# Optimization experiments

Hardware: AMD Instinct MI355X
Metric: run time of the kernel (lower is better)

Reference implementation:

```python
import jax, jax.numpy as jnp
import numpy as np

NUM_HEADS = 8

def setup_inputs() -> dict:
    key = jax.random.key(0)
    ks = jax.random.split(key, 12)
    B, C, H, W = 4, 256, 64, 64
    QK = 256
    NSP = 256
    x = jax.random.normal(ks[0], (B, C, H, W), dtype=jnp.float32)
    affinity_matrix = jax.random.uniform(ks[1], (B, NSP, H * W), dtype=jnp.float32)
    norm_w = 1.0 + 0.02 * jax.random.normal(ks[2], (C,), dtype=jnp.float32)
    norm_b = 0.02 * jax.random.normal(ks[3], (C,), dtype=jnp.float32)
    Wq = 0.02 * jax.random.normal(ks[4], (QK, C), dtype=jnp.float32)
    Wk = 0.02 * jax.random.normal(ks[5], (QK, C), dtype=jnp.float32)
    Wv = 0.02 * jax.random.normal(ks[6], (C, C), dtype=jnp.float32)
    Wsp = 0.02 * jax.random.normal(ks[7], (QK, C), dtype=jnp.float32)
    lepe_w = 0.02 * jax.random.normal(ks[8], (C, 1, 3, 3), dtype=jnp.float32)  # depthwise OIHW
    lepe_b = 0.02 * jax.random.normal(ks[9], (C,), dtype=jnp.float32)
    return {"x": x, "affinity_matrix": affinity_matrix, "norm_w": norm_w,
            "norm_b": norm_b, "Wq": Wq, "Wk": Wk, "Wv": Wv, "Wsp": Wsp,
            "lepe_w": lepe_w, "lepe_b": lepe_b, "num_spixels": NSP}


def _layernorm2d(x, w, b, eps=1e-6):
    # LayerNorm over channel dim of NCHW input
    xp = x.transpose(0, 2, 3, 1)  # B,H,W,C
    mu = xp.mean(-1, keepdims=True)
    var = ((xp - mu) ** 2).mean(-1, keepdims=True)
    xn = (xp - mu) * jax.lax.rsqrt(var + eps) * w + b
    return xn.transpose(0, 3, 1, 2)


def _sgca(x, affinity_matrix, norm_w, norm_b, Wq, Wk, Wv, Wsp, lepe_w, lepe_b, num_spixels):
    B, C, H, W = x.shape
    HW = H * W
    h = NUM_HEADS
    qk_dim = Wq.shape[0]
    dqk = qk_dim // h
    dv = C // h
    scale = (C // h) ** -0.5

    xn = _layernorm2d(x, norm_w, norm_b)

    # superpixel aggregation: b (hw) c
    x_flat = xn.reshape(B, C, HW).transpose(0, 2, 1)  # B,HW,C
    stoken = jnp.einsum('bmn,bnc->bmc', affinity_matrix, x_flat)
    stoken = stoken / (affinity_matrix.sum(-1, keepdims=True) + 1e-16)  # B,nsp,C

    # sp projection -> B,h,dqk,nsp
    st = jnp.einsum('bmc,qc->bmq', stoken, Wsp).transpose(0, 2, 1)
    st = st.reshape(B, h, dqk, num_spixels)

    # 1x1 conv projections
    q = jnp.einsum('oc,bchw->bohw', Wq, xn).reshape(B, h, dqk, HW)
    k = jnp.einsum('oc,bchw->bohw', Wk, xn).reshape(B, h, dqk, HW)
    vx = jnp.einsum('oc,bchw->bohw', Wv, xn)  # B,C,H,W
    v = vx.reshape(B, h, dv, HW)

    # LePE: depthwise 3x3 conv on v(x)
    lepe = jax.lax.conv_general_dilated(
        vx, lepe_w, window_strides=(1, 1), padding=((1, 1), (1, 1)),
        feature_group_count=C, dimension_numbers=('NCHW', 'OIHW', 'NCHW'))
    lepe = lepe + lepe_b[None, :, None, None]
    # faithful to original: [B,C,HW] -> permute -> [B,HW,C] -> reshape B,C,H,W
    lepe = lepe.reshape(B, C, HW).transpose(0, 2, 1).reshape(B, C, H, W)

    # stage 1: k^T @ stoken, softmax over HW axis
    s_attn = jnp.einsum('bhdn,bhdm->bhnm', k, st) * scale  # B,h,HW,nsp
    s_attn = jax.nn.softmax(s_attn, axis=-2)
    s_out = jnp.einsum('bhdn,bhnm->bhdm', v, s_attn)  # B,h,dv,nsp

    # stage 2: stoken^T @ q, softmax over nsp axis
    x_attn = jnp.einsum('bhdm,bhdn->bhmn', st, q) * scale  # B,h,nsp,HW
    x_attn = jax.nn.softmax(x_attn, axis=-2)
    x_out = jnp.einsum('bhdm,bhmn->bhdn', s_out, x_attn).reshape(B, C, H, W)

    return x_out + lepe


def reference(x, affinity_matrix, norm_w, norm_b, Wq, Wk, Wv, Wsp, lepe_w, lepe_b, num_spixels):
    return _sgca(x, affinity_matrix, norm_w, norm_b, Wq, Wk, Wv, Wsp, lepe_w, lepe_b, num_spixels)
```

## Files before the change

kernel.cpp:

```cpp
#include <hip/hip_runtime.h>
#include <hip/hip_bf16.h>

#define BATCH 4
#define CCH   256
#define HWHW  4096
#define NSP   256
#define NHEAD 8
#define SCALE 0.17677669529663689f
#define PLANE 1048576L

typedef short bf16x8 __attribute__((ext_vector_type(8)));
typedef short bf16x4 __attribute__((ext_vector_type(4)));
typedef float f32x4  __attribute__((ext_vector_type(4)));

__device__ __forceinline__ short f2bs(float f) {
    __hip_bfloat16 h = __float2bfloat16(f);
    return *(short*)&h;
}
__device__ __forceinline__ bf16x8 cvt8(float4 a, float4 b) {
    bf16x8 p;
    p[0] = f2bs(a.x); p[1] = f2bs(a.y); p[2] = f2bs(a.z); p[3] = f2bs(a.w);
    p[4] = f2bs(b.x); p[5] = f2bs(b.y); p[6] = f2bs(b.z); p[7] = f2bs(b.w);
    return p;
}
__device__ __forceinline__ void gll16(const __hip_bfloat16* g, __hip_bfloat16* l) {
    __builtin_amdgcn_global_load_lds(
        (const __attribute__((address_space(1))) unsigned int*)(const void*)g,
        (__attribute__((address_space(3))) unsigned int*)(void*)l,
        16, 0, 0);
}

__global__ __launch_bounds__(512)
void ln_fused_kernel(const float* __restrict__ x, const float* __restrict__ w,
                     const float* __restrict__ bb,
                     const float* __restrict__ Wq, const float* __restrict__ Wk,
                     const float* __restrict__ Wv, const float* __restrict__ Wsp,
                     __hip_bfloat16* __restrict__ xn_cn,
                     __hip_bfloat16* __restrict__ xn_nc,
                     __hip_bfloat16* __restrict__ wbf)
{
    __shared__ float ps[32][64], pss[32][64];
    __shared__ float mus[64], rstds[64];
    __shared__ float wls[256], bls[256];
    int blk = blockIdx.x;
    int t = threadIdx.x;
    if (blk >= 256) {
        int sel = blk - 256;
        const float* src = (sel == 0) ? Wq : (sel == 1) ? Wk : (sel == 2) ? Wv : Wsp;
        __hip_bfloat16* dst = wbf + sel * 65536;
        for (int i = t * 4; i < 65536; i += 2048) {
            float4 f = *(const float4*)(src + i);
            __hip_bfloat16 p[4];
            p[0] = __float2bfloat16(f.x); p[1] = __float2bfloat16(f.y);
            p[2] = __float2bfloat16(f.z); p[3] = __float2bfloat16(f.w);
            *(int2*)(dst + i) = *(int2*)p;
        }
        return;
    }
    int b = blk >> 6;
    int n0 = (blk & 63) * 64;
    int pg = t & 15;
    int cq = t >> 4;
    if (t < 256) { wls[t] = w[t]; bls[t] = bb[t]; }

    const float* xp = x + ((long)(b * CCH + cq * 8)) * HWHW + n0 + pg * 4;
    float4 v[8];
#pragma unroll
    for (int i = 0; i < 8; ++i) v[i] = *(const float4*)(xp + (long)i * HWHW);
    float4 s = {0.f,0.f,0.f,0.f}, ss = {0.f,0.f,0.f,0.f};
#pragma unroll
    for (int i = 0; i < 8; ++i) {
        s.x += v[i].x; s.y += v[i].y; s.z += v[i].z; s.w += v[i].w;
        ss.x += v[i].x * v[i].x; ss.y += v[i].y * v[i].y;
        ss.z += v[i].z * v[i].z; ss.w += v[i].w * v[i].w;
    }
    *(float4*)&ps[cq][pg * 4]  = s;
    *(float4*)&pss[cq][pg * 4] = ss;
    __syncthreads();
    if (t < 64) {
        float S = 0.f, SS = 0.f;
#pragma unroll
        for (int q = 0; q < 32; ++q) { S += ps[q][t]; SS += pss[q][t]; }
        float mu = S * (1.f / 256.f);
        float var = SS * (1.f / 256.f) - mu * mu;
        mus[t] = mu; rstds[t] = rsqrtf(var + 1e-6f);
    }
    __syncthreads();
    float4 mu4 = *(float4*)&mus[pg * 4];
    float4 rs4 = *(float4*)&rstds[pg * 4];

    bf16x8 pk[4];
#pragma unroll
    for (int i = 0; i < 8; ++i) {
        int c = cq * 8 + i;
        float wc = wls[c], bc = bls[c];
        short h0 = f2bs((v[i].x - mu4.x) * rs4.x * wc + bc);
        short h1 = f2bs((v[i].y - mu4.y) * rs4.y * wc + bc);
        short h2 = f2bs((v[i].z - mu4.z) * rs4.z * wc + bc);
        short h3 = f2bs((v[i].w - mu4.w) * rs4.w * wc + bc);
        pk[0][i] = h0; pk[1][i] = h1; pk[2][i] = h2; pk[3][i] = h3;
        bf16x4 q; q[0] = h0; q[1] = h1; q[2] = h2; q[3] = h3;
        *(bf16x4*)(xn_cn + ((long)(b * CCH + c)) * HWHW + n0 + pg * 4) = q;
    }
#pragma unroll
    for (int j = 0; j < 4; ++j)
        *(bf16x8*)(xn_nc + ((long)b * HWHW + n0 + pg * 4 + j) * CCH + cq * 8) = pk[j];
}

__device__ __forceinline__ void gemm_k256_128(
    const __hip_bfloat16* __restrict__ A, const __hip_bfloat16* __restrict__ B,
    __hip_bfloat16* __restrict__ C, int bx, int by, int bz,
    int N, long aStrideZ, long bStrideZ, long cStrideZ,
    __hip_bfloat16* __restrict__ Asm)
{
    const int K = 256;
    const int t = threadIdx.x, lane = t & 63, w = t >> 6;
    const int l15 = lane & 15, quad = lane >> 4;
    const int Mt = by * 128, Nt = bx * 128;
    {
        const __hip_bfloat16* aBase = A + (long)bz * aStrideZ
            + (long)(Mt + l15) * K + quad * 8;
#pragma unroll
        for (int p = 0; p < 16; ++p) {
            const int rt = w * 2 + (p >> 3), s = p & 7;
            gll16(aBase + (long)(rt * 16) * K + s * 32, Asm + (rt * 8 + s) * 512);
        }
    }
    const int wm2 = w & 1, wn2 = w >> 1;
    const __hip_bfloat16* bBase = B + (long)bz * bStrideZ
        + (long)(Nt + wn2 * 64 + l15) * K + quad * 8;

    f32x4 acc[4][4];
#pragma unroll
    for (int mi = 0; mi < 4; ++mi)
#pragma unroll
        for (int nj = 0; nj < 4; ++nj) acc[mi][nj] = f32x4{0.f,0.f,0.f,0.f};

    bf16x8 bEv[4], bOd[4];
#pragma unroll
    for (int nj = 0; nj < 4; ++nj)
        bEv[nj] = *(const bf16x8*)(bBase + (long)(nj * 16) * K);
    __syncthreads();
#pragma unroll
    for (int sp = 0; sp < 4; ++sp) {
        const int s0 = 2 * sp, s1 = 2 * sp + 1;
#pragma unroll
        for (int nj = 0; nj < 4; ++nj)
            bOd[nj] = *(const bf16x8*)(bBase + (long)(nj * 16) * K + s1 * 32);
#pragma unroll
        for (int mi = 0; mi < 4; ++mi) {
            bf16x8 a = *(const bf16x8*)&Asm[((wm2 * 4 + mi) * 8 + s0) * 512 + lane * 8];
            acc[mi][0] = __builtin_amdgcn_mfma_f32_16x16x32_bf16(a, bEv[0], acc[mi][0], 0, 0, 0);
            acc[mi][1] = __builtin_amdgcn_mfma_f32_16x16x32_bf16(a, bEv[1], acc[mi][1], 0, 0, 0);
            acc[mi][2] = __builtin_amdgcn_mfma_f32_16x16x32_bf16(a, bEv[2], acc[mi][2], 0, 0, 0);
            acc[mi][3] = __builtin_amdgcn_mfma_f32_16x16x32_bf16(a, bEv[3], acc[mi][3], 0, 0, 0);
        }
        if (sp < 3) {
#pragma unroll
            for (int nj = 0; nj < 4; ++nj)
                bEv[nj] = *(const bf16x8*)(bBase + (long)(nj * 16) * K + (s0 + 2) * 32);
        }
#pragma unroll
        for (int mi = 0; mi < 4; ++mi) {
            bf16x8 a = *(const bf16x8*)&Asm[((wm2 * 4 + mi) * 8 + s1) * 512 + lane * 8];
            acc[mi][0] = __builtin_amdgcn_mfma_f32_16x16x32_bf16(a, bOd[0], acc[mi][0], 0, 0, 0);
            acc[mi][1] = __builtin_amdgcn_mfma_f32_16x16x32_bf16(a, bOd[1], acc[mi][1], 0, 0, 0);
            acc[mi][2] = __builtin_amdgcn_mfma_f32_16x16x32_bf16(a, bOd[2], acc[mi][2], 0, 0, 0);
            acc[mi][3] = __builtin_amdgcn_mfma_f32_16x16x32_bf16(a, bOd[3], acc[mi][3], 0, 0, 0);
        }
    }
#pragma unroll
    for (int mi = 0; mi < 4; ++mi)
#pragma unroll
        for (int nj = 0; nj < 4; ++nj)
#pragma unroll
            for (int r = 0; r < 4; ++r) {
                int m = Mt + wm2 * 64 + mi * 16 + quad * 4 + r;
                int n = Nt + wn2 * 64 + nj * 16 + l15;
                C[(long)bz * cStrideZ + (long)m * N + n] =
                    __float2bfloat16(acc[mi][nj][r]);
            }
}

template <int OUTK, int ASTAGE, bool ROWSUM, int NTL>
__device__ __forceinline__ void gemm_body(
    const void* __restrict__ Av, const __hip_bfloat16* __restrict__ B,
    void* __restrict__ Cptr, int bx, int by, int bz,
    int N, int K, int kChunk, int kShift,
    long aStrideZ, long bStrideZ, long cStrideZ,
    float* __restrict__ rsPart,
    __hip_bfloat16* __restrict__ Asm, __hip_bfloat16* __restrict__ Bsm,
    float* __restrict__ rsl)
{
    int z = bz;
    int b = z >> kShift;
    int ch = z & ((1 << kShift) - 1);
    int t = threadIdx.x;
    int lane = t & 63, w = t >> 6;
    int l15 = lane & 15, quad = lane >> 4;
    int Mt = by * 64, Nt = bx * 64 * NTL;

    if (ASTAGE == 2 && t < 64) {
        float s = 0.f;
#pragma unroll
        for (int pl = 0; pl < 8; ++pl) s += rsPart[((b * 8 + pl) << 8) + Mt + t];
        rsl[t] = s;
    }

    long aOff = (long)b * aStrideZ + (long)ch * kChunk
        + (long)(Mt + w * 16 + l15) * K + quad * 8;
    const float* aSrcF = (const float*)Av + aOff;
    const __hip_bfloat16* bSrc = B + (long)b * bStrideZ + (long)ch * kChunk
        + (long)(Nt + w * 16 + l15) * K + quad * 8;

    f32x4 acc[NTL][2][2];
#pragma unroll
    for (int nt = 0; nt < NTL; ++nt)
#pragma unroll
        for (int i = 0; i < 2; ++i)
#pragma unroll
            for (int j = 0; j < 2; ++j) acc[nt][i][j] = f32x4{0.f,0.f,0.f,0.f};
    f32x4 rs0 = {0.f,0.f,0.f,0.f}, rs1 = rs0;
    bf16x8 onesf;
    { short o = (l15 == 0) ? (short)0x3F80 : (short)0;
      onesf = bf16x8{o, o, o, o, o, o, o, o}; }
    int wm = (w & 1) * 2, wn = (w >> 1) * 2;

    float4 pf0, pf1, pf2, pf3;
    if (ASTAGE == 1) {
        pf0 = *(const float4*)(aSrcF);      pf1 = *(const float4*)(aSrcF + 4);
        pf2 = *(const float4*)(aSrcF + 32); pf3 = *(const float4*)(aSrcF + 36);
    }

    const bf16x8* AsmU = (const bf16x8*)Asm;
    const bf16x8* BsmU = (const bf16x8*)Bsm;

    for (int k0 = 0; k0 < kChunk; k0 += 64) {
        if (ASTAGE == 1) {
            *(bf16x8*)&Asm[t * 8]        = cvt8(pf0, pf1);
            *(bf16x8*)&Asm[2048 + t * 8] = cvt8(pf2, pf3);
        } else {
#pragma unroll
            for (int kh = 0; kh < 2; ++kh) {
                float4 s0 = {0.f,0.f,0.f,0.f}, s1 = {0.f,0.f,0.f,0.f};
#pragma unroll
                for (int pl = 0; pl < 8; ++pl) {
                    const float* p = aSrcF + (long)pl * 65536 + k0 + kh * 32;
                    float4 u0 = *(const float4*)p, u1 = *(const float4*)(p + 4);
                    s0.x += u0.x; s0.y += u0.y; s0.z += u0.z; s0.w += u0.w;
                    s1.x += u1.x; s1.y += u1.y; s1.z += u1.z; s1.w += u1.w;
                }
                *(bf16x8*)&Asm[kh * 2048 + t * 8] = cvt8(s0, s1);
            }
        }
#pragma unroll
        for (int nt = 0; nt < NTL; ++nt) {
            gll16(bSrc + (long)nt * 64 * K + k0,      Bsm + nt * 4096 + w * 512);
            gll16(bSrc + (long)nt * 64 * K + k0 + 32, Bsm + nt * 4096 + 2048 + w * 512);
        }
        __syncthreads();
        if (ASTAGE == 1 && k0 + 64 < kChunk) {
            const float* nx = aSrcF + k0 + 64;
            pf0 = *(const float4*)nx;        pf1 = *(const float4*)(nx + 4);
            pf2 = *(const float4*)(nx + 32); pf3 = *(const float4*)(nx + 36);
        }
#pragma unroll
        for (int kh = 0; kh < 2; ++kh) {
            bf16x8 a0 = AsmU[kh * 256 + wm * 64 + lane];
            bf16x8 a1 = AsmU[kh * 256 + (wm + 1) * 64 + lane];
            if (ROWSUM) {
                rs0 = __builtin_amdgcn_mfma_f32_16x16x32_bf16(a0, onesf, rs0, 0, 0, 0);
                rs1 = __builtin_amdgcn_mfma_f32_16x16x32_bf16(a1, onesf, rs1, 0, 0, 0);
            }
#pragma unroll
            for (int nt = 0; nt < NTL; ++nt) {
                bf16x8 b0 = BsmU[nt * 512 + kh * 256 + wn * 64 + lane];
                bf16x8 b1 = BsmU[nt * 512 + kh * 256 + (wn + 1) * 64 + lane];
                acc[nt][0][0] = __builtin_amdgcn_mfma_f32_16x16x32_bf16(a0, b0, acc[nt][0][0], 0, 0, 0);
                acc[nt][0][1] = __builtin_amdgcn_mfma_f32_16x16x32_bf16(a0, b1, acc[nt][0][1], 0, 0, 0);
                acc[nt][1][0] = __builtin_amdgcn_mfma_f32_16x16x32_bf16(a1, b0, acc[nt][1][0], 0, 0, 0);
                acc[nt][1][1] = __builtin_amdgcn_mfma_f32_16x16x32_bf16(a1, b1, acc[nt][1][1], 0, 0, 0);
            }
        }
        __syncthreads();
    }
    if (ROWSUM && bx == 0 && (w >> 1) == 0 && l15 == 0) {
#pragma unroll
        for (int r = 0; r < 4; ++r) {
            rsPart[(long)z * 256 + Mt + wm * 16 + quad * 4 + r]       = rs0[r];
            rsPart[(long)z * 256 + Mt + (wm + 1) * 16 + quad * 4 + r] = rs1[r];
        }
    }
#pragma unroll
    for (int nt = 0; nt < NTL; ++nt)
#pragma unroll
        for (int i = 0; i < 2; ++i)
#pragma unroll
            for (int j = 0; j < 2; ++j)
#pragma unroll
                for (int r = 0; r < 4; ++r) {
                    int m = Mt + (wm + i) * 16 + quad * 4 + r;
                    int n = Nt + nt * 64 + (wn + j) * 16 + l15;
                    float val = acc[nt][i][j][r];
                    if (ASTAGE == 2) val /= (rsl[m - Mt] + 1e-16f);
                    long off = (long)z * cStrideZ + (long)m * N + n;
                    if (OUTK == 0) ((float*)Cptr)[off] = val;
                    else ((__hip_bfloat16*)Cptr)[off] = __float2bfloat16(val);
                }
}

__global__ __launch_bounds__(256, 2)
void mega1_kernel(const float* __restrict__ aff,
                  const __hip_bfloat16* __restrict__ xn_cn,
                  const __hip_bfloat16* __restrict__ xn_nc,
                  const __hip_bfloat16* __restrict__ wbf,
                  __hip_bfloat16* __restrict__ qk_nc,
                  __hip_bfloat16* __restrict__ v_cn,
                  float* __restrict__ stoken_part,
                  float* __restrict__ rs_part)
{
    __shared__ __align__(16) char smem[65536];
    __hip_bfloat16* Asm = (__hip_bfloat16*)smem;
    __hip_bfloat16* Bsm = (__hip_bfloat16*)(smem + 8192);
    __hip_bfloat16* A128 = (__hip_bfloat16*)smem;
    int blk = blockIdx.x;
    if (blk < 128) {
        int i = blk;
        gemm_body<0, 1, true, 4>(aff, xn_cn, stoken_part,
            0, i >> 5, i & 31, 256, 4096, 512, 3,
            PLANE, PLANE, 65536L, rs_part, Asm, Bsm, nullptr);
    } else if (blk < 640) {
        int i = blk - 128;
        int bx = i >> 7, rem = i & 127;
        gemm_k256_128(xn_nc, wbf, qk_nc,
            bx, rem >> 2, rem & 3, 512, PLANE, 0L, 2 * PLANE, A128);
    } else {
        int i = blk - 640;
        int by = i >> 7, rem = i & 127;
        gemm_k256_128(wbf + 2 * 65536, xn_nc, v_cn,
            rem >> 2, by, rem & 3, 4096, 0L, PLANE, PLANE, A128);
    }
}

__device__ __forceinline__
void lepe_dev(char* smem, int bx, int cy, int b,
              const __hip_bfloat16* __restrict__ v_cn,
              const float* __restrict__ lw, const float* __restrict__ lb,
              __hip_bfloat16* __restrict__ lepe_cn)
{
    __hip_bfloat16* in_t    = (__hip_bfloat16*)smem;
    __hip_bfloat16* tile_bf = (__hip_bfloat16*)(smem + 24576);
    float* wls = (float*)(smem + 41472);
    float* bls = (float*)(smem + 42624);
    const int c0 = cy * 32;
    const int t = threadIdx.x;
    const int n0 = bx * 256, r0 = bx * 4;

    for (int i = t; i < 288; i += 256) wls[i] = lw[c0 * 9 + i];
    if (t < 32)  bls[t] = lb[c0 + t];
#pragma unroll
    for (int i = 0; i < 6; ++i) {
        int vi = t + i * 256;
        int ch = vi / 48;
        int off = (vi % 48) * 8;
        int g = (r0 - 1) * 64 + off;
        int4 val = {0, 0, 0, 0};
        if ((unsigned)g < 4096u)
            val = *(const int4*)(v_cn + (((long)(b * CCH + c0 + ch)) << 12) + g);
        *(int4*)&in_t[ch * 384 + off] = val;
    }
    __syncthreads();

    const int lane = t & 63, w = t >> 6;
#pragma unroll
    for (int i = 0; i < 8; ++i) {
        int ch = w * 8 + i;
        float cr[6], lf[6], rf[6];
#pragma unroll
        for (int rr = 0; rr < 6; ++rr) {
            cr[rr] = (float)in_t[ch * 384 + rr * 64 + lane];
            float lv = __shfl_up(cr[rr], 1);
            float rv = __shfl_down(cr[rr], 1);
            lf[rr] = (lane == 0) ? 0.f : lv;
            rf[rr] = (lane == 63) ? 0.f : rv;
        }
        float w0 = wls[ch*9+0], w1 = wls[ch*9+1], w2 = wls[ch*9+2];
        float w3 = wls[ch*9+3], w4 = wls[ch*9+4], w5 = wls[ch*9+5];
        float w6 = wls[ch*9+6], w7 = wls[ch*9+7], w8 = wls[ch*9+8];
        float bias = bls[ch];
#pragma unroll
        for (int r = 0; r < 4; ++r) {
            float acc = bias
                + lf[r]   * w0 + cr[r]   * w1 + rf[r]   * w2
                + lf[r+1] * w3 + cr[r+1] * w4 + rf[r+1] * w5
                + lf[r+2] * w6 + cr[r+2] * w7 + rf[r+2] * w8;
            tile_bf[(r * 64 + lane) * 33 + ch] = __float2bfloat16(acc);
        }
    }
    __syncthreads();
#pragma unroll
    for (int i = 0; i < 32; ++i) {
        int idx = t + i * 256;
        int nl = idx >> 5, cj = idx & 31;
        int sp = n0 + nl;
        lepe_cn[((long)(b * CCH + (sp >> 4)) << 12) + (nl & 15) * 256 + c0 + cj] =
            tile_bf[nl * 33 + cj];
    }
}

__global__ __launch_bounds__(256)
void stmd_lepe_kernel(const float* __restrict__ part,
                      const __hip_bfloat16* __restrict__ wsp,
                      __hip_bfloat16* __restrict__ st_md,
                      float* __restrict__ rs_part,
                      const __hip_bfloat16* __restrict__ v_cn,
                      const float* __restrict__ lw, const float* __restrict__ lb,
                      __hip_bfloat16* __restrict__ lepe_cn)
{
    __shared__ __align__(16) char smem[43008];
    int blk = blockIdx.x;
    if (blk < 64) {
        __hip_bfloat16* Asm = (__hip_bfloat16*)smem;
        __hip_bfloat16* Bsm = (__hip_bfloat16*)(smem + 8192);
        float* rsl = (float*)(smem + 16384);
        int i = blk;
        gemm_body<1, 2, false, 1>(part, wsp, st_md,
            i & 3, (i >> 2) & 3, i >> 4, 256, 256, 256, 0,
            524288L, 0L, 65536L, rs_part, Asm, Bsm, rsl);
    } else {
        int j = blk - 64;
        lepe_dev(smem, j & 15, (j >> 4) & 7, j >> 7, v_cn, lw, lb, lepe_cn);
    }
}

__global__ __launch_bounds__(256)
void mega2_kernel(const __hip_bfloat16* __restrict__ qk_nc,
                  const __hip_bfloat16* __restrict__ v_cn,
                  const __hip_bfloat16* __restrict__ st_md,
                  __hip_bfloat16* __restrict__ opart)
{
    __shared__ __align__(16) char smem[36864];
    __hip_bfloat16* Es  = (__hip_bfloat16*)smem;
    __hip_bfloat16* sts = (__hip_bfloat16*)smem;
    const int chunk = blockIdx.x & 15, bh = blockIdx.x >> 4;
    const int b = bh >> 3, h = bh & 7;
    const int t = threadIdx.x, lane = t & 63, w = t >> 6;
    const int l15 = lane & 15, quad = lane >> 4;
    const int n0 = chunk * 256;

    {
        const int4* src = (const int4*)(st_md + ((long)(b * 256 + t)) * 256 + h * 32);
        int4* dst = (int4*)&sts[t * 40];
        dst[0] = src[0]; dst[1] = src[1]; dst[2] = src[2]; dst[3] = src[3];
    }
    const __hip_bfloat16* kfp = qk_nc + ((long)b * 4096 + n0 + 16 * w + l15) * 512 + 256 + h * 32 + quad * 8;
    const __hip_bfloat16* vp0 = v_cn + ((long)(b * 256 + h * 32 + l15)) * 4096 + n0 + quad * 8;
    const __hip_bfloat16* vp1 = vp0 + 16 * 4096;
    bf16x8 kfs[4], vv[4][4];
    kfs[0]   = *(const bf16x8*)(kfp);
    vv[0][0] = *(const bf16x8*)(vp0);
    vv[0][1] = *(const bf16x8*)(vp1);
    vv[0][2] = *(const bf16x8*)(vp0 + 32);
    vv[0][3] = *(const bf16x8*)(vp1 + 32);
    __syncthreads();
    bf16x8 afrag[16];
#pragma unroll
    for (int mt = 0; mt < 16; ++mt)
        afrag[mt] = *(const bf16x8*)&sts[(mt * 16 + l15) * 40 + quad * 8];
    __syncthreads();
    bf16x8 onesf;
    { short o = (l15 == 0) ? (short)0x3F80 : (short)0;
      onesf = bf16x8{o, o, o, o, o, o, o, o}; }

    f32x4 occ[4][3];
#pragma unroll
    for (int i = 0; i < 4; ++i)
#pragma unroll
        for (int j = 0; j < 3; ++j) occ[i][j] = f32x4{0.f,0.f,0.f,0.f};

#pragma unroll
    for (int sub = 0; sub < 4; ++sub) {
#pragma unroll
        for (int mt = 0; mt < 16; ++mt) {
            f32x4 s = __builtin_amdgcn_mfma_f32_16x16x32_bf16(afrag[mt], kfs[sub], f32x4{0.f,0.f,0.f,0.f}, 0, 0, 0);
#pragma unroll
            for (int r = 0; r < 4; ++r)
                Es[(mt * 16 + quad * 4 + r) * 72 + 16 * w + l15] =
                    __float2bfloat16(__expf(s[r] * SCALE));
        }
        if (sub < 3) {
            kfs[sub + 1]   = *(const bf16x8*)(kfp + (long)(sub + 1) * 64 * 512);
            vv[sub + 1][0] = *(const bf16x8*)(vp0 + (sub + 1) * 64);
            vv[sub + 1][1] = *(const bf16x8*)(vp1 + (sub + 1) * 64);
            vv[sub + 1][2] = *(const bf16x8*)(vp0 + (sub + 1) * 64 + 32);
            vv[sub + 1][3] = *(const bf16x8*)(vp1 + (sub + 1) * 64 + 32);
        }
        __syncthreads();
#pragma unroll
        for (int ks = 0; ks < 2; ++ks) {
            bf16x8 bf0 = vv[sub][2 * ks + 0];
            bf16x8 bf1 = vv[sub][2 * ks + 1];
#pragma unroll
            for (int mi = 0; mi < 4; ++mi) {
                bf16x8 af = *(const bf16x8*)&Es[(64 * w + mi * 16 + l15) * 72 + ks * 32 + quad * 8];
                occ[mi][0] = __builtin_amdgcn_mfma_f32_16x16x32_bf16(af, bf0, occ[mi][0], 0, 0, 0);
                occ[mi][1] = __builtin_amdgcn_mfma_f32_16x16x32_bf16(af, bf1, occ[mi][1], 0, 0, 0);
                occ[mi][2] = __builtin_amdgcn_mfma_f32_16x16x32_bf16(af, onesf, occ[mi][2], 0, 0, 0);
            }
        }
        __syncthreads();
    }
    __hip_bfloat16* tb = Es;
#pragma unroll
    for (int mi = 0; mi < 4; ++mi)
#pragma unroll
        for (int jt = 0; jt < 3; ++jt) {
            if (jt == 2 && l15 != 0) continue;
            int col = jt * 16 + l15;
#pragma unroll
            for (int r = 0; r < 4; ++r) {
                int m = 64 * w + mi * 16 + quad * 4 + r;
                tb[col * 264 + m] = __float2bfloat16(occ[mi][jt][r]);
            }
        }
    __syncthreads();
    int* og = (int*)(opart) + (long)(chunk * 32 + bh) * 4224;
    const int* tbi = (const int*)tb;
#pragma unroll
    for (int i = 0; i < 17; ++i) {
        int idx = t + i * 256;
        if (idx < 4224) {
            int row = idx >> 7, off = idx & 127;
            og[idx] = tbi[row * 132 + off];
        }
    }
}

__global__ __launch_bounds__(256)
void merge1_kernel(const __hip_bfloat16* __restrict__ opart, __hip_bfloat16* __restrict__ sout)
{
    int t = blockIdx.x * 256 + threadIdx.x;
    int m = t & 255;
    int d = (t >> 8) & 31;
    int bh = t >> 13;
    float num = 0.f, den = 0.f;
    for (int ch = 0; ch < 16; ++ch) {
        long base = (long)((ch * 32 + bh) * 33) * 256 + m;
        num += (float)opart[base + (long)d * 256];
        den += (float)opart[base + 32 * 256];
    }
    sout[(long)bh * 8192 + d * 256 + m] = __float2bfloat16(num / den);
}

__global__ __launch_bounds__(256)
void stage2_mfma(const __hip_bfloat16* __restrict__ qk_nc,
                 const __hip_bfloat16* __restrict__ st_md,
                 const __hip_bfloat16* __restrict__ sout_bf,
                 const __hip_bfloat16* __restrict__ lepe_cn,
                 float* __restrict__ out)
{
    __shared__ __align__(16) char smem[50688];
    __hip_bfloat16* Es2 = (__hip_bfloat16*)smem;
    __hip_bfloat16* sos = (__hip_bfloat16*)(smem + 33792);
    float* o_t = (float*)smem;
    const int chunk = blockIdx.x, bh = blockIdx.y;
    const int b = bh >> 3, h = bh & 7;
    const int t = threadIdx.x, lane = t & 63, w = t >> 6;
    const int l15 = lane & 15, quad = lane >> 4;
    const int n0 = chunk * 256;

    {
        int row = t >> 3, seg = t & 7;
        const int4* src = (const int4*)(sout_bf + (long)bh * 8192 + row * 256 + seg * 32);
        int4* dst = (int4*)&sos[row * 264 + seg * 32];
        dst[0] = src[0]; dst[1] = src[1]; dst[2] = src[2]; dst[3] = src[3];
    }
    bf16x8 stfrag[4];
#pragma unroll
    for (int mt = 0; mt < 4; ++mt)
        stfrag[mt] = *(const bf16x8*)(st_md
            + ((long)(b * 256 + 64 * w + mt * 16 + l15)) * 256 + h * 32 + quad * 8);
    const __hip_bfloat16* qfp = qk_nc + ((long)b * 4096 + n0 + l15) * 512 + h * 32 + quad * 8;
    bf16x8 qq[4][4];
#pragma unroll
    for (int nt = 0; nt < 4; ++nt)
        qq[0][nt] = *(const bf16x8*)(qfp + (long)(nt * 16) * 512);
    bf16x8 onesf;
    { short o = (l15 == 0) ? (short)0x3F80 : (short)0;
      onesf = bf16x8{o, o, o, o, o, o, o, o}; }
    __syncthreads();

#pragma unroll
    for (int sub = 0; sub < 4; ++sub) {
        const int nbase = n0 + sub * 64;
#pragma unroll
        for (int nt = 0; nt < 4; ++nt) {
            bf16x8 qf = qq[sub][nt];
#pragma unroll
            for (int mt = 0; mt < 4; ++mt) {
                f32x4 s = __builtin_amdgcn_mfma_f32_16x16x32_bf16(qf, stfrag[mt], f32x4{0.f,0.f,0.f,0.f}, 0, 0, 0);
#pragma unroll
                for (int r = 0; r < 4; ++r)
                    Es2[(nt * 16 + quad * 4 + r) * 264 + 64 * w + mt * 16 + l15] =
                        __float2bfloat16(__expf(s[r] * SCALE));
            }
        }
        if (sub < 3) {
#pragma unroll
            for (int nt = 0; nt < 4; ++nt)
                qq[sub + 1][nt] = *(const bf16x8*)(qfp + (long)((sub + 1) * 64 + nt * 16) * 512);
        }
        __syncthreads();
        f32x4 o0 = {0.f,0.f,0.f,0.f}, o1 = o0, o2 = o0;
#pragma unroll
        for (int ks = 0; ks < 8; ++ks) {
            bf16x8 af = *(const bf16x8*)&Es2[(16 * w + l15) * 264 + ks * 32 + quad * 8];
            bf16x8 b0 = *(const bf16x8*)&sos[(l15) * 264 + ks * 32 + quad * 8];
            bf16x8 b1 = *(const bf16x8*)&sos[(16 + l15) * 264 + ks * 32 + quad * 8];
            o0 = __builtin_amdgcn_mfma_f32_16x16x32_bf16(af, b0, o0, 0, 0, 0);
            o1 = __builtin_amdgcn_mfma_f32_16x16x32_bf16(af, b1, o1, 0, 0, 0);
            o2 = __builtin_amdgcn_mfma_f32_16x16x32_bf16(af, onesf, o2, 0, 0, 0);
        }
        __syncthreads();
#pragma unroll
        for (int r = 0; r < 4; ++r) {
            float den = __shfl(o2[r], lane & 48);
            float inv = 1.f / den;
            o_t[(l15) * 68 + 16 * w + quad * 4 + r]      = o0[r] * inv;
            o_t[(16 + l15) * 68 + 16 * w + quad * 4 + r] = o1[r] * inv;
        }
        __syncthreads();
        {
            int row = t >> 3, coff = (t & 7) * 8;
            long gb = ((long)(b * 256 + h * 32 + row)) * 4096 + nbase + coff;
            int4 lp4 = *(const int4*)(lepe_cn + gb);
            const __hip_bfloat16* lp = (const __hip_bfloat16*)&lp4;
            const float* sp = &o_t[row * 68 + coff];
            float4 r0, r1;
            r0.x = sp[0] + (float)lp[0]; r0.y = sp[1] + (float)lp[1];
            r0.z = sp[2] + (float)lp[2]; r0.w = sp[3] + (float)lp[3];
            r1.x = sp[4] + (float)lp[4]; r1.y = sp[5] + (float)lp[5];
            r1.z = sp[6] + (float)lp[6]; r1.w = sp[7] + (float)lp[7];
            *(float4*)(out + gb)     = r0;
            *(float4*)(out + gb + 4) = r1;
        }
        __syncthreads();
    }
}

extern "C" void kernel_launch(void* const* d_in, const int* in_sizes, int n_in,
                              void* d_out, int out_size, void* d_ws, size_t ws_size,
                              hipStream_t stream)
{
    const float* x    = (const float*)d_in[0];
    const float* aff  = (const float*)d_in[1];
    const float* nw   = (const float*)d_in[2];
    const float* nb   = (const float*)d_in[3];
    const float* Wq   = (const float*)d_in[4];
    const float* Wk   = (const float*)d_in[5];
    const float* Wv   = (const float*)d_in[6];
    const float* Wsp  = (const float*)d_in[7];
    const float* lw   = (const float*)d_in[8];
    const float* lb   = (const float*)d_in[9];
    float* out = (float*)d_out;

    float* ws = (float*)d_ws;
    const long P = PLANE;
    __hip_bfloat16* qk_nc  = (__hip_bfloat16*)(ws);
    __hip_bfloat16* v_cn   = (__hip_bfloat16*)(ws + 4 * P);
    __hip_bfloat16* xn_cn  = (__hip_bfloat16*)(ws + 6 * P);
    __hip_bfloat16* xn_nc  = (__hip_bfloat16*)(ws + 8 * P);
    __hip_bfloat16* lepe_cn= (__hip_bfloat16*)(ws + 10 * P);
    float* stoken_part = ws + 14 * P;
    __hip_bfloat16* opart = (__hip_bfloat16*)(ws + 16 * P);
    float* tail        = ws + 16 * P + 2162688;
    __hip_bfloat16* wbf       = (__hip_bfloat16*)tail;
    __hip_bfloat16* st_md     = (__hip_bfloat16*)(tail + 262144);
    __hip_bfloat16* sout_bf   = (__hip_bfloat16*)(tail + 393216);
    float* rs_part = tail + 525312;

    ln_fused_kernel<<<260, 512, 0, stream>>>(x, nw, nb, Wq, Wk, Wv, Wsp,
                                             xn_cn, xn_nc, wbf);
    mega1_kernel<<<896, 256, 0, stream>>>(aff, xn_cn, xn_nc, wbf,
                                          qk_nc, v_cn, stoken_part, rs_part);
    stmd_lepe_kernel<<<576, 256, 0, stream>>>(stoken_part, wbf + 3 * 65536,
                                              st_md, rs_part,
                                              v_cn, lw, lb, lepe_cn);
    mega2_kernel<<<512, 256, 0, stream>>>(qk_nc, v_cn, st_md, opart);
    merge1_kernel<<<1024, 256, 0, stream>>>(opart, sout_bf);
    stage2_mfma<<<dim3(16, 32), 256, 0, stream>>>(qk_nc, st_md, sout_bf, lepe_cn, out);
}
```

Baseline: 189.4 us.

## Split stage-1 superpixel rows and stage-2 HW chunks to double block counts

mega2 now splits the 256 superpixels into two halves per block, so there are twice as many blocks, each with half the LDS and registers. Each block writes its half into the shared partial buffer. stage2 processes 128 spatial positions per block instead of 256, which also doubles its grid. The aim is to raise occupancy and wave count on the many-CU GPU, at the cost of redundant K/V and st loads across the extra blocks.

```diff
diff --git a/kernel.cpp b/kernel.cpp
--- a/kernel.cpp
+++ b/kernel.cpp
@@ -439,70 +439,69 @@
                   const __hip_bfloat16* __restrict__ st_md,
                   __hip_bfloat16* __restrict__ opart)
 {
-    __shared__ __align__(16) char smem[36864];
+    __shared__ __align__(16) char smem[18432];
     __hip_bfloat16* Es  = (__hip_bfloat16*)smem;
     __hip_bfloat16* sts = (__hip_bfloat16*)smem;
-    const int chunk = blockIdx.x & 15, bh = blockIdx.x >> 4;
+    const int blk = blockIdx.x;
+    const int mh = blk & 1;
+    const int chunk = (blk >> 1) & 15;
+    const int bh = blk >> 5;
     const int b = bh >> 3, h = bh & 7;
     const int t = threadIdx.x, lane = t & 63, w = t >> 6;
     const int l15 = lane & 15, quad = lane >> 4;
     const int n0 = chunk * 256;
 
     {
-        const int4* src = (const int4*)(st_md + ((long)(b * 256 + t)) * 256 + h * 32);
-        int4* dst = (int4*)&sts[t * 40];
-        dst[0] = src[0]; dst[1] = src[1]; dst[2] = src[2]; dst[3] = src[3];
+        int row = t >> 1, half = t & 1;
+        const int4* src = (const int4*)(st_md
+            + ((long)(b * 256 + mh * 128 + row)) * 256 + h * 32 + half * 16);
+        int4* dst = (int4*)&sts[row * 40 + half * 16];
+        dst[0] = src[0]; dst[1] = src[1];
     }
     const __hip_bfloat16* kfp = qk_nc + ((long)b * 4096 + n0 + 16 * w + l15) * 512 + 256 + h * 32 + quad * 8;
     const __hip_bfloat16* vp0 = v_cn + ((long)(b * 256 + h * 32 + l15)) * 4096 + n0 + quad * 8;
     const __hip_bfloat16* vp1 = vp0 + 16 * 4096;
-    bf16x8 kfs[4], vv[4][4];
-    kfs[0]   = *(const bf16x8*)(kfp);
-    vv[0][0] = *(const bf16x8*)(vp0);
-    vv[0][1] = *(const bf16x8*)(vp1);
-    vv[0][2] = *(const bf16x8*)(vp0 + 32);
-    vv[0][3] = *(const bf16x8*)(vp1 + 32);
-    __syncthreads();
-    bf16x8 afrag[16];
-#pragma unroll
-    for (int mt = 0; mt < 16; ++mt)
+    bf16x8 kfc = *(const bf16x8*)(kfp);
+    __syncthreads();
+    bf16x8 afrag[8];
+#pragma unroll
+    for (int mt = 0; mt < 8; ++mt)
         afrag[mt] = *(const bf16x8*)&sts[(mt * 16 + l15) * 40 + quad * 8];
     __syncthreads();
     bf16x8 onesf;
     { short o = (l15 == 0) ? (short)0x3F80 : (short)0;
       onesf = bf16x8{o, o, o, o, o, o, o, o}; }
 
-    f32x4 occ[4][3];
-#pragma unroll
-    for (int i = 0; i < 4; ++i)
+    f32x4 occ[2][3];
+#pragma unroll
+    for (int i = 0; i < 2; ++i)
 #pragma unroll
         for (int j = 0; j < 3; ++j) occ[i][j] = f32x4{0.f,0.f,0.f,0.f};
 
 #pragma unroll
     for (int sub = 0; sub < 4; ++sub) {
-#pragma unroll
-        for (int mt = 0; mt < 16; ++mt) {
-            f32x4 s = __builtin_amdgcn_mfma_f32_16x16x32_bf16(afrag[mt], kfs[sub], f32x4{0.f,0.f,0.f,0.f}, 0, 0, 0);
+        bf16x8 vv0 = *(const bf16x8*)(vp0 + sub * 64);
+        bf16x8 vv1 = *(const bf16x8*)(vp1 + sub * 64);
+        bf16x8 vv2 = *(const bf16x8*)(vp0 + sub * 64 + 32);
+        bf16x8 vv3 = *(const bf16x8*)(vp1 + sub * 64 + 32);
+#pragma unroll
+        for (int mt = 0; mt < 8; ++mt) {
+            f32x4 s = __builtin_amdgcn_mfma_f32_16x16x32_bf16(afrag[mt], kfc, f32x4{0.f,0.f,0.f,0.f}, 0, 0, 0);
 #pragma unroll
             for (int r = 0; r < 4; ++r)
                 Es[(mt * 16 + quad * 4 + r) * 72 + 16 * w + l15] =
                     __float2bfloat16(__expf(s[r] * SCALE));
         }
-        if (sub < 3) {
-            kfs[sub + 1]   = *(const bf16x8*)(kfp + (long)(sub + 1) * 64 * 512);
-            vv[sub + 1][0] = *(const bf16x8*)(vp0 + (sub + 1) * 64);
-            vv[sub + 1][1] = *(const bf16x8*)(vp1 + (sub + 1) * 64);
-            vv[sub + 1][2] = *(const bf16x8*)(vp0 + (sub + 1) * 64 + 32);
-            vv[sub + 1][3] = *(const bf16x8*)(vp1 + (sub + 1) * 64 + 32);
-        }
+        if (sub < 3)
+            kfc = *(const bf16x8*)(kfp + (long)(sub + 1) * 64 * 512);
         __syncthreads();
 #pragma unroll
         for (int ks = 0; ks < 2; ++ks) {
-            bf16x8 bf0 = vv[sub][2 * ks + 0];
-            bf16x8 bf1 = vv[sub][2 * ks + 1];
-#pragma unroll
-            for (int mi = 0; mi < 4; ++mi) {
-                bf16x8 af = *(const bf16x8*)&Es[(64 * w + mi * 16 + l15) * 72 + ks * 32 + quad * 8];
+            bf16x8 bf0 = (ks == 0) ? vv0 : vv2;
+            bf16x8 bf1 = (ks == 0) ? vv1 : vv3;
+#pragma unroll
+            for (int mi = 0; mi < 2; ++mi) {
+                bf16x8 af = *(const bf16x8*)&Es[(32 * w + mi * 16 + l15) * 72 + ks * 32 + quad * 8];
                 occ[mi][0] = __builtin_amdgcn_mfma_f32_16x16x32_bf16(af, bf0, occ[mi][0], 0, 0, 0);
                 occ[mi][1] = __builtin_amdgcn_mfma_f32_16x16x32_bf16(af, bf1, occ[mi][1], 0, 0, 0);
                 occ[mi][2] = __builtin_amdgcn_mfma_f32_16x16x32_bf16(af, onesf, occ[mi][2], 0, 0, 0);
@@ -512,26 +511,26 @@
     }
     __hip_bfloat16* tb = Es;
 #pragma unroll
-    for (int mi = 0; mi < 4; ++mi)
+    for (int mi = 0; mi < 2; ++mi)
 #pragma unroll
         for (int jt = 0; jt < 3; ++jt) {
             if (jt == 2 && l15 != 0) continue;
             int col = jt * 16 + l15;
 #pragma unroll
             for (int r = 0; r < 4; ++r) {
-                int m = 64 * w + mi * 16 + quad * 4 + r;
-                tb[col * 264 + m] = __float2bfloat16(occ[mi][jt][r]);
+                int m = 32 * w + mi * 16 + quad * 4 + r;
+                tb[col * 136 + m] = __float2bfloat16(occ[mi][jt][r]);
             }
         }
     __syncthreads();
     int* og = (int*)(opart) + (long)(chunk * 32 + bh) * 4224;
     const int* tbi = (const int*)tb;
 #pragma unroll
-    for (int i = 0; i < 17; ++i) {
+    for (int i = 0; i < 9; ++i) {
         int idx = t + i * 256;
-        if (idx < 4224) {
-            int row = idx >> 7, off = idx & 127;
-            og[idx] = tbi[row * 132 + off];
+        if (idx < 2112) {
+            int row = idx >> 6, off = idx & 63;
+            og[row * 128 + mh * 64 + off] = tbi[row * 68 + off];
         }
     }
 }
@@ -567,7 +566,7 @@
     const int b = bh >> 3, h = bh & 7;
     const int t = threadIdx.x, lane = t & 63, w = t >> 6;
     const int l15 = lane & 15, quad = lane >> 4;
-    const int n0 = chunk * 256;
+    const int n0 = chunk * 128;
 
     {
         int row = t >> 3, seg = t & 7;
@@ -581,7 +580,7 @@
         stfrag[mt] = *(const bf16x8*)(st_md
             + ((long)(b * 256 + 64 * w + mt * 16 + l15)) * 256 + h * 32 + quad * 8);
     const __hip_bfloat16* qfp = qk_nc + ((long)b * 4096 + n0 + l15) * 512 + h * 32 + quad * 8;
-    bf16x8 qq[4][4];
+    bf16x8 qq[2][4];
 #pragma unroll
     for (int nt = 0; nt < 4; ++nt)
         qq[0][nt] = *(const bf16x8*)(qfp + (long)(nt * 16) * 512);
@@ -591,7 +590,7 @@
     __syncthreads();
 
 #pragma unroll
-    for (int sub = 0; sub < 4; ++sub) {
+    for (int sub = 0; sub < 2; ++sub) {
         const int nbase = n0 + sub * 64;
 #pragma unroll
         for (int nt = 0; nt < 4; ++nt) {
@@ -605,10 +604,10 @@
                         __float2bfloat16(__expf(s[r] * SCALE));
             }
         }
-        if (sub < 3) {
+        if (sub < 1) {
 #pragma unroll
             for (int nt = 0; nt < 4; ++nt)
-                qq[sub + 1][nt] = *(const bf16x8*)(qfp + (long)((sub + 1) * 64 + nt * 16) * 512);
+                qq[1][nt] = *(const bf16x8*)(qfp + (long)(64 + nt * 16) * 512);
         }
         __syncthreads();
         f32x4 o0 = {0.f,0.f,0.f,0.f}, o1 = o0, o2 = o0;
@@ -686,7 +685,7 @@
     stmd_lepe_kernel<<<576, 256, 0, stream>>>(stoken_part, wbf + 3 * 65536,
                                               st_md, rs_part,
                                               v_cn, lw, lb, lepe_cn);
-    mega2_kernel<<<512, 256, 0, stream>>>(qk_nc, v_cn, st_md, opart);
+    mega2_kernel<<<1024, 256, 0, stream>>>(qk_nc, v_cn, st_md, opart);
     merge1_kernel<<<1024, 256, 0, stream>>>(opart, sout_bf);
-    stage2_mfma<<<dim3(16, 32), 256, 0, stream>>>(qk_nc, st_md, sout_bf, lepe_cn, out);
-}
+    stage2_mfma<<<dim3(32, 32), 256, 0, stream>>>(qk_nc, st_md, sout_bf, lepe_cn, out);
+}
```

Result: no change. 187.6 us (-0.9%).
